# Kernel optimization log

Hardware: AMD Instinct MI355X
Metric: run time of the kernel (lower is better)

The kernel has to match this reference:

```python
import jax, jax.numpy as jnp
import numpy as np

B, N, D, H, WIN = 8, 4096, 768, 8, 8
HD = D // H
FG = N // 2 + 1
FL = WIN // 2 + 1


def _gelu(x):
    return jax.nn.gelu(x, approximate=False)


def _cgelu(z):
    # magnitude-based complex GELU: z * gelu(|z|) / (|z| + 1e-6)
    mag = jnp.abs(z)
    return z * (_gelu(mag) / (mag + 1e-6))


def setup_inputs():
    key = jax.random.key(0)
    ks = jax.random.split(key, 8)

    def w(k, shape):
        return jax.random.normal(k, shape, dtype=jnp.float32) * 0.02

    return {
        "x": jax.random.normal(ks[0], (B, N, D), dtype=jnp.float32),
        "ln_w": jnp.ones((D,), jnp.float32),
        "ln_b": jnp.zeros((D,), jnp.float32),
        "bf_g": jnp.ones((H, FG, 1), jnp.float32),
        "bb_g": jnp.full((H, FG, 1), -0.1, jnp.float32),
        "bf_l": jnp.ones((H, FL, 1), jnp.float32),
        "bb_l": jnp.full((H, FL, 1), -0.1, jnp.float32),
        "w1g": w(ks[1], (D, D)),
        "b1g": jnp.zeros((D,), jnp.float32),
        "w2g": w(ks[2], (D, H * FG * 2)),
        "b2g": jnp.zeros((H * FG * 2,), jnp.float32),
        "w1l": w(ks[3], (D, D)),
        "b1l": jnp.zeros((D,), jnp.float32),
        "w2l": w(ks[4], (D, H * FL * 2)),
        "b2l": jnp.zeros((H * FL * 2,), jnp.float32),
        "wf1": w(ks[5], (D, D // 2)),
        "bf1": jnp.zeros((D // 2,), jnp.float32),
        "wf2": w(ks[6], (D // 2, H)),
        "bf2": jnp.zeros((H,), jnp.float32),
    }


def reference(x, ln_w, ln_b, bf_g, bb_g, bf_l, bb_l, w1g, b1g, w2g, b2g,
              w1l, b1l, w2l, b2l, wf1, bf1, wf2, bf2):
    # pre-norm (LayerNorm, eps=1e-5)
    mu = jnp.mean(x, axis=-1, keepdims=True)
    var = jnp.mean((x - mu) ** 2, axis=-1, keepdims=True)
    xn = (x - mu) / jnp.sqrt(var + 1e-5) * ln_w + ln_b
    xh = xn.reshape(B, N, H, HD).transpose(0, 2, 1, 3)  # (B,H,N,HD)
    ctx = xn.mean(axis=1)  # (B,D)

    # ---- global branch: Hann-windowed rFFT over full sequence ----
    ag = (_gelu(ctx @ w1g + b1g) @ w2g + b2g).reshape(B, H, FG, 2)
    hann_g = jnp.hanning(N).astype(x.dtype)[None, None, :, None]
    Ff = jnp.fft.rfft(xh * hann_g, axis=2, norm="ortho")  # (B,H,FG,HD) complex
    eff_f = bf_g[None] * (1.0 + ag[..., 0:1])
    eff_b = bb_g[None] + ag[..., 1:2]
    x_global = jnp.fft.irfft(_cgelu(Ff * eff_f + eff_b), n=N, axis=2, norm="ortho")

    al = (_gelu(ctx @ w1l + b1l) @ w2l + b2l).reshape(B, H, FL, 2)
    nw = N // WIN
    hann_l = jnp.hanning(WIN).astype(x.dtype)[None, None, None, :, None]
    xw = xh.reshape(B, H, nw, WIN, HD) * hann_l
    Fl_fft = jnp.fft.rfft(xw, axis=3, norm="ortho")  # (B,H,nw,FL,HD)
    eff_fl = bf_l[None, :, None] * (1.0 + al[:, :, None, :, 0:1])
    eff_bl = bb_l[None, :, None] + al[:, :, None, :, 1:2]
    x_local = jnp.fft.irfft(_cgelu(Fl_fft * eff_fl + eff_bl), n=WIN, axis=3,
                            norm="ortho").reshape(B, H, N, HD)

    # ---- fusion gate ----
    alpha = jax.nn.sigmoid(_gelu(ctx @ wf1 + bf1) @ wf2 + bf2).reshape(B, H, 1, 1)
    fused = alpha * x_global + (1.0 - alpha) * x_local
    return x + fused.transpose(0, 2, 1, 3).reshape(B, N, D)
```

## Files before the change

### kernel.cpp

```cpp
#include <hip/hip_runtime.h>
#include <math.h>

#define B_ 8
#define N_ 4096
#define D_ 768
#define H_ 8
#define HD_ 96
#define FG_ 2049
#define TWO_PI 6.283185307179586476925f
#define PAD(i) ((i) + ((i) >> 5))

__device__ __forceinline__ float erf_fast(float x) {
    float ax = fabsf(x);
    float t = __builtin_amdgcn_rcpf(fmaf(0.3275911f, ax, 1.0f));
    float p = fmaf(fmaf(fmaf(fmaf(1.061405429f, t, -1.453152027f), t, 1.421413741f),
                        t, -0.284496736f), t, 0.254829592f) * t;
    float r = 1.0f - p * __expf(-ax * ax);
    return copysignf(r, x);
}

__device__ __forceinline__ float gelu_f(float x) {
    return 0.5f * x * (1.0f + erf_fast(x * 0.7071067811865475f));
}

__device__ __forceinline__ int rev4_12(int x) {
    int r = (int)(__brev((unsigned)x) >> 20);
    return ((r & 0x555) << 1) | ((r >> 1) & 0x555);
}

__global__ void k_init(const float* __restrict__ b2g, const float* __restrict__ b2l,
                       float2* __restrict__ twg, float* __restrict__ hanng,
                       float* __restrict__ ctx, float* __restrict__ ag,
                       float* __restrict__ al) {
    int i = blockIdx.x * 256 + threadIdx.x;
    if (i < 2048) {
        float s, c;
        sincosf(-TWO_PI * (float)i / 4096.0f, &s, &c);
        twg[i] = make_float2(c, s);
    }
    if (i < 4096) hanng[i] = 0.5f - 0.5f * cosf(TWO_PI * (float)i / 4095.0f);
    if (i < B_ * D_) ctx[i] = 0.f;
    const int CG = H_ * FG_ * 2;
    if (i < CG) {
        float v = b2g[i];
        for (int b = 0; b < B_; ++b) ag[(size_t)b * CG + i] = v;
    } else if (i < CG + 80) {
        int cc = i - CG;
        float v = b2l[cc];
        for (int b = 0; b < B_; ++b) al[b * 80 + cc] = v;
    }
}

__global__ __launch_bounds__(256) void k_stats(const float* __restrict__ x,
                                               float* __restrict__ mu,
                                               float* __restrict__ rstd) {
    int row = blockIdx.x * 4 + (threadIdx.x >> 6);
    int lane = threadIdx.x & 63;
    const float4* xr = (const float4*)(x + (size_t)row * D_);
    float4 a = xr[lane], b = xr[lane + 64], c = xr[lane + 128];
    float s = a.x + a.y + a.z + a.w + b.x + b.y + b.z + b.w + c.x + c.y + c.z + c.w;
    #pragma unroll
    for (int o = 32; o > 0; o >>= 1) s += __shfl_xor(s, o);
    float m = s * (1.0f / 768.0f);
    float v = 0.f, d;
    d = a.x - m; v += d * d; d = a.y - m; v += d * d;
    d = a.z - m; v += d * d; d = a.w - m; v += d * d;
    d = b.x - m; v += d * d; d = b.y - m; v += d * d;
    d = b.z - m; v += d * d; d = b.w - m; v += d * d;
    d = c.x - m; v += d * d; d = c.y - m; v += d * d;
    d = c.z - m; v += d * d; d = c.w - m; v += d * d;
    #pragma unroll
    for (int o = 32; o > 0; o >>= 1) v += __shfl_xor(v, o);
    if (lane == 0) {
        mu[row] = m;
        rstd[row] = rsqrtf(v * (1.0f / 768.0f) + 1e-5f);
    }
}

__global__ __launch_bounds__(256) void k_lnT(const float* __restrict__ x,
                                             const float* __restrict__ mu,
                                             const float* __restrict__ rstd,
                                             const float* __restrict__ lw,
                                             const float* __restrict__ lb,
                                             float* __restrict__ xt,
                                             float* __restrict__ ctx) {
    __shared__ float tile[64][65];
    __shared__ float csum[4][64];
    int d0 = blockIdx.x * 64, n0 = blockIdx.y * 64, b = blockIdx.z;
    int c = threadIdx.x & 63, r4 = threadIdx.x >> 6;
    float w = lw[d0 + c], bias = lb[d0 + c];
    float partial = 0.f;
    #pragma unroll
    for (int q = 0; q < 16; ++q) {
        int r = r4 * 16 + q;
        int row = b * N_ + n0 + r;
        float v = (x[(size_t)row * D_ + d0 + c] - mu[row]) * rstd[row] * w + bias;
        tile[r][c] = v;
        partial += v;
    }
    csum[r4][c] = partial;
    __syncthreads();
    if (r4 == 0)
        atomicAdd(ctx + b * D_ + d0 + c,
                  (csum[0][c] + csum[1][c] + csum[2][c] + csum[3][c]) * (1.0f / 4096.0f));
    #pragma unroll
    for (int q = 0; q < 16; ++q) {
        int r = r4 * 16 + q;
        xt[((size_t)b * D_ + d0 + r) * N_ + n0 + c] = tile[c][r];
    }
}

__global__ void k_mlp1(const float* __restrict__ ctx,
                       const float* __restrict__ w1g, const float* __restrict__ b1g,
                       const float* __restrict__ w1l, const float* __restrict__ b1l,
                       const float* __restrict__ wf1, const float* __restrict__ bf1,
                       float* __restrict__ h1g, float* __restrict__ h1l, float* __restrict__ hf) {
    __shared__ float cl[B_ * D_];
    for (int i = threadIdx.x; i < B_ * D_; i += 256) cl[i] = ctx[i];
    __syncthreads();
    int c = blockIdx.x * 256 + threadIdx.x;
    if (c >= 1920) return;
    const float *w, *bias; float* out; int ncol, cc;
    if (c < 768)      { w = w1g; bias = b1g; out = h1g; ncol = 768; cc = c; }
    else if (c < 1536){ w = w1l; bias = b1l; out = h1l; ncol = 768; cc = c - 768; }
    else              { w = wf1; bias = bf1; out = hf;  ncol = 384; cc = c - 1536; }
    float acc[B_];
    #pragma unroll
    for (int b = 0; b < B_; ++b) acc[b] = 0.f;
    for (int d = 0; d < 768; ++d) {
        float wv = w[(size_t)d * ncol + cc];
        #pragma unroll
        for (int b = 0; b < B_; ++b) acc[b] += cl[b * 768 + d] * wv;
    }
    float bv = bias[cc];
    for (int b = 0; b < B_; ++b) out[b * ncol + cc] = gelu_f(acc[b] + bv);
}

__global__ void k_mlp2(const float* __restrict__ h1g, const float* __restrict__ h1l,
                       const float* __restrict__ hf,
                       const float* __restrict__ w2g, const float* __restrict__ w2l,
                       const float* __restrict__ wf2, const float* __restrict__ bf2,
                       float* __restrict__ ag, float* __restrict__ al, float* __restrict__ gate) {
    int kc = blockIdx.y;
    int d0 = kc * 96;
    __shared__ float lg[B_ * 96];
    __shared__ float ll[B_ * 96];
    for (int i = threadIdx.x; i < B_ * 96; i += 256) {
        int bb = i / 96, dd = i % 96;
        lg[i] = h1g[bb * 768 + d0 + dd];
        ll[i] = h1l[bb * 768 + d0 + dd];
    }
    __syncthreads();
    int c = blockIdx.x * 256 + threadIdx.x;
    const int CG = H_ * FG_ * 2;
    float acc[B_];
    #pragma unroll
    for (int b = 0; b < B_; ++b) acc[b] = 0.f;
    if (c < CG) {
        for (int d = 0; d < 96; ++d) {
            float wv = w2g[(size_t)(d0 + d) * CG + c];
            #pragma unroll
            for (int b = 0; b < B_; ++b) acc[b] += lg[b * 96 + d] * wv;
        }
        for (int b = 0; b < B_; ++b) atomicAdd(ag + (size_t)b * CG + c, acc[b]);
    } else if (c < CG + 80) {
        int cc = c - CG;
        for (int d = 0; d < 96; ++d) {
            float wv = w2l[(d0 + d) * 80 + cc];
            #pragma unroll
            for (int b = 0; b < B_; ++b) acc[b] += ll[b * 96 + d] * wv;
        }
        for (int b = 0; b < B_; ++b) atomicAdd(al + b * 80 + cc, acc[b]);
    } else if (c < CG + 88 && kc == 0) {
        int cc = c - CG - 80;
        for (int d = 0; d < 384; ++d) {
            float wv = wf2[d * 8 + cc];
            #pragma unroll
            for (int b = 0; b < B_; ++b) acc[b] += hf[b * 384 + d] * wv;
        }
        for (int b = 0; b < B_; ++b)
            gate[b * 8 + cc] = 1.0f / (1.0f + expf(-(acc[b] + bf2[cc])));
    }
}

template<int LQ>
__device__ __forceinline__ void dif_stage(float2* z, const float2* __restrict__ twg, int t) {
    const int Q = 1 << LQ;
    #pragma unroll
    for (int u = 0; u < 4; ++u) {
        int j = t + (u << 8);
        int pos = j & (Q - 1);
        int i0 = ((j >> LQ) << (LQ + 2)) + pos;
        int p0 = PAD(i0), p1 = PAD(i0 + Q), p2 = PAD(i0 + 2 * Q), p3 = PAD(i0 + 3 * Q);
        float2 a = z[p0], bq = z[p1], c = z[p2], d = z[p3];
        float t0x = a.x + c.x,  t0y = a.y + c.y;
        float t1x = a.x - c.x,  t1y = a.y - c.y;
        float t2x = bq.x + d.x, t2y = bq.y + d.y;
        float t3x = bq.x - d.x, t3y = bq.y - d.y;
        float2 w1 = twg[pos << (10 - LQ)];
        float2 w2 = make_float2(w1.x * w1.x - w1.y * w1.y, 2.f * w1.x * w1.y);
        float2 w3 = make_float2(w1.x * w2.x - w1.y * w2.y, w1.x * w2.y + w1.y * w2.x);
        z[p0] = make_float2(t0x + t2x, t0y + t2y);
        float y1x = t1x + t3y, y1y = t1y - t3x;
        z[p1] = make_float2(y1x * w1.x - y1y * w1.y, y1x * w1.y + y1y * w1.x);
        float y2x = t0x - t2x, y2y = t0y - t2y;
        z[p2] = make_float2(y2x * w2.x - y2y * w2.y, y2x * w2.y + y2y * w2.x);
        float y3x = t1x - t3y, y3y = t1y + t3x;
        z[p3] = make_float2(y3x * w3.x - y3y * w3.y, y3x * w3.y + y3y * w3.x);
    }
}

template<int LQ>
__device__ __forceinline__ void dit_stage(float2* z, const float2* __restrict__ twg, int t) {
    const int Q = 1 << LQ;
    #pragma unroll
    for (int u = 0; u < 4; ++u) {
        int j = t + (u << 8);
        int pos = j & (Q - 1);
        int i0 = ((j >> LQ) << (LQ + 2)) + pos;
        int p0 = PAD(i0), p1 = PAD(i0 + Q), p2 = PAD(i0 + 2 * Q), p3 = PAD(i0 + 3 * Q);
        float2 a = z[p0], bq = z[p1], c = z[p2], d = z[p3];
        float2 w1 = twg[pos << (10 - LQ)];
        w1.y = -w1.y;
        float2 w2 = make_float2(w1.x * w1.x - w1.y * w1.y, 2.f * w1.x * w1.y);
        float2 w3 = make_float2(w1.x * w2.x - w1.y * w2.y, w1.x * w2.y + w1.y * w2.x);
        float2 bh = make_float2(bq.x * w1.x - bq.y * w1.y, bq.x * w1.y + bq.y * w1.x);
        float2 ch = make_float2(c.x * w2.x - c.y * w2.y, c.x * w2.y + c.y * w2.x);
        float2 dh = make_float2(d.x * w3.x - d.y * w3.y, d.x * w3.y + d.y * w3.x);
        float t0x = a.x + ch.x,  t0y = a.y + ch.y;
        float t1x = a.x - ch.x,  t1y = a.y - ch.y;
        float t2x = bh.x + dh.x, t2y = bh.y + dh.y;
        float t3x = bh.x - dh.x, t3y = bh.y - dh.y;
        z[p0] = make_float2(t0x + t2x, t0y + t2y);
        z[p1] = make_float2(t1x - t3y, t1y + t3x);
        z[p2] = make_float2(t0x - t2x, t0y - t2y);
        z[p3] = make_float2(t1x + t3y, t1y - t3x);
    }
}

#define W16C_INIT {1.f, 0.9238795325f, 0.7071067812f, 0.3826834324f, 0.f, \
                   -0.3826834324f, -0.7071067812f, -0.9238795325f, -1.f, -0.9238795325f}
#define W16S_INIT {0.f, -0.3826834324f, -0.7071067812f, -0.9238795325f, -1.f, \
                   -0.9238795325f, -0.7071067812f, -0.3826834324f, 0.f, 0.3826834324f}

__device__ __forceinline__ void fwd16(float2* v) {
    const float WC[10] = W16C_INIT;
    const float WS[10] = W16S_INIT;
    #pragma unroll
    for (int n0 = 0; n0 < 4; ++n0) {
        float2 a = v[n0], b = v[n0 + 4], c = v[n0 + 8], d = v[n0 + 12];
        float t0x = a.x + c.x, t0y = a.y + c.y, t1x = a.x - c.x, t1y = a.y - c.y;
        float t2x = b.x + d.x, t2y = b.y + d.y, t3x = b.x - d.x, t3y = b.y - d.y;
        v[n0] = make_float2(t0x + t2x, t0y + t2y);
        float y1x = t1x + t3y, y1y = t1y - t3x;
        float y2x = t0x - t2x, y2y = t0y - t2y;
        float y3x = t1x - t3y, y3y = t1y + t3x;
        v[n0 + 4]  = make_float2(y1x * WC[n0] - y1y * WS[n0], y1x * WS[n0] + y1y * WC[n0]);
        v[n0 + 8]  = make_float2(y2x * WC[2*n0] - y2y * WS[2*n0], y2x * WS[2*n0] + y2y * WC[2*n0]);
        v[n0 + 12] = make_float2(y3x * WC[3*n0] - y3y * WS[3*n0], y3x * WS[3*n0] + y3y * WC[3*n0]);
    }
    #pragma unroll
    for (int g = 0; g < 4; ++g) {
        float2 a = v[4*g], b = v[4*g+1], c = v[4*g+2], d = v[4*g+3];
        float t0x = a.x + c.x, t0y = a.y + c.y, t1x = a.x - c.x, t1y = a.y - c.y;
        float t2x = b.x + d.x, t2y = b.y + d.y, t3x = b.x - d.x, t3y = b.y - d.y;
        v[4*g]   = make_float2(t0x + t2x, t0y + t2y);
        v[4*g+1] = make_float2(t1x + t3y, t1y - t3x);
        v[4*g+2] = make_float2(t0x - t2x, t0y - t2y);
        v[4*g+3] = make_float2(t1x - t3y, t1y + t3x);
    }
}

__device__ __forceinline__ void inv16(float2* v) {
    const float WC[10] = W16C_INIT;
    const float WS[10] = W16S_INIT;
    #pragma unroll
    for (int g = 0; g < 4; ++g) {
        float2 a = v[4*g], b = v[4*g+1], c = v[4*g+2], d = v[4*g+3];
        float t0x = a.x + c.x, t0y = a.y + c.y, t1x = a.x - c.x, t1y = a.y - c.y;
        float t2x = b.x + d.x, t2y = b.y + d.y, t3x = b.x - d.x, t3y = b.y - d.y;
        v[4*g]   = make_float2(t0x + t2x, t0y + t2y);
        v[4*g+1] = make_float2(t1x - t3y, t1y + t3x);
        v[4*g+2] = make_float2(t0x - t2x, t0y - t2y);
        v[4*g+3] = make_float2(t1x + t3y, t1y - t3x);
    }
    #pragma unroll
    for (int n0 = 0; n0 < 4; ++n0) {
        float2 a = v[n0];
        float2 b0 = v[n0 + 4], c0 = v[n0 + 8], dd = v[n0 + 12];
        float2 b = make_float2(b0.x * WC[n0] + b0.y * WS[n0], b0.y * WC[n0] - b0.x * WS[n0]);
        float2 c = make_float2(c0.x * WC[2*n0] + c0.y * WS[2*n0], c0.y * WC[2*n0] - c0.x * WS[2*n0]);
        float2 d = make_float2(dd.x * WC[3*n0] + dd.y * WS[3*n0], dd.y * WC[3*n0] - dd.x * WS[3*n0]);
        float t0x = a.x + c.x, t0y = a.y + c.y, t1x = a.x - c.x, t1y = a.y - c.y;
        float t2x = b.x + d.x, t2y = b.y + d.y, t3x = b.x - d.x, t3y = b.y - d.y;
        v[n0]      = make_float2(t0x + t2x, t0y + t2y);
        v[n0 + 4]  = make_float2(t1x - t3y, t1y + t3x);
        v[n0 + 8]  = make_float2(t0x - t2x, t0y - t2y);
        v[n0 + 12] = make_float2(t1x + t3y, t1y - t3x);
    }
}

__global__ __launch_bounds__(256) void k_spectral(
        const float* __restrict__ xt,
        const float* __restrict__ ag,
        const float* __restrict__ al,
        const float* __restrict__ gate,
        const float* __restrict__ bf_g, const float* __restrict__ bb_g,
        const float* __restrict__ bf_l, const float* __restrict__ bb_l,
        const float2* __restrict__ twg, const float* __restrict__ hanng,
        float* __restrict__ fused)
{
    __shared__ float2 z[4224];
    int line0 = blockIdx.x * 2;
    int d0 = line0 % 768, b = line0 / 768;
    int h = d0 / HD_;
    int t = threadIdx.x;

    const float* src0 = xt + (size_t)line0 * N_;
    const float* src1 = src0 + N_;
    float raw0[16], raw1[16];
    #pragma unroll
    for (int q = 0; q < 4; ++q) {
        float4 v0 = ((const float4*)src0)[t * 4 + q];
        float4 v1 = ((const float4*)src1)[t * 4 + q];
        raw0[q * 4 + 0] = v0.x; raw0[q * 4 + 1] = v0.y;
        raw0[q * 4 + 2] = v0.z; raw0[q * 4 + 3] = v0.w;
        raw1[q * 4 + 0] = v1.x; raw1[q * 4 + 1] = v1.y;
        raw1[q * 4 + 2] = v1.z; raw1[q * 4 + 3] = v1.w;
    }
    #pragma unroll
    for (int q = 0; q < 4; ++q) {
        float4 hw = ((const float4*)hanng)[t * 4 + q];
        int nb = t * 16 + q * 4;
        z[PAD(nb + 0)] = make_float2(raw0[q * 4 + 0] * hw.x, raw1[q * 4 + 0] * hw.x);
        z[PAD(nb + 1)] = make_float2(raw0[q * 4 + 1] * hw.y, raw1[q * 4 + 1] * hw.y);
        z[PAD(nb + 2)] = make_float2(raw0[q * 4 + 2] * hw.z, raw1[q * 4 + 2] * hw.z);
        z[PAD(nb + 3)] = make_float2(raw0[q * 4 + 3] * hw.w, raw1[q * 4 + 3] * hw.w);
    }

    float alc = gate[b * 8 + h];
    const float* alb = al + b * 80;
    float effl_f[5], effl_b[5];
    #pragma unroll
    for (int f = 0; f < 5; ++f) {
        int idx = h * 5 + f;
        effl_f[f] = bf_l[idx] * (1.0f + alb[idx * 2]);
        effl_b[f] = bb_l[idx] + alb[idx * 2 + 1];
    }
    const float s8 = 0.3535533905932738f;
    const float c7 = 0.7071067811865476f;
    const float cosT[8] = {1.f, c7, 0.f, -c7, -1.f, -c7, 0.f, c7};
    const float sinT[8] = {0.f, c7, 1.f, c7, 0.f, -c7, -1.f, -c7};
    const float hl[8] = {0.f, 0.18825510f, 0.61126047f, 0.95048444f,
                         0.95048444f, 0.61126047f, 0.18825510f, 0.f};
    float xl0[16], xl1[16];
    #pragma unroll
    for (int ln = 0; ln < 2; ++ln) {
        float* rawp = ln ? raw1 : raw0;
        float* xlp  = ln ? xl1 : xl0;
        #pragma unroll
        for (int w2 = 0; w2 < 2; ++w2) {
            float xw[8];
            #pragma unroll
            for (int j = 0; j < 8; ++j) xw[j] = rawp[w2 * 8 + j] * hl[j];
            float Yr[5], Yi[5];
            #pragma unroll
            for (int f = 0; f < 5; ++f) {
                float fr = 0.f, fi = 0.f;
                #pragma unroll
                for (int j = 0; j < 8; ++j) {
                    int k8 = (f * j) & 7;
                    fr += xw[j] * cosT[k8];
                    fi -= xw[j] * sinT[k8];
                }
                fr *= s8; fi *= s8;
                float zr = fr * effl_f[f] + effl_b[f];
                float zi = fi * effl_f[f];
                float mag = sqrtf(zr * zr + zi * zi);
                float g = gelu_f(mag) * __builtin_amdgcn_rcpf(mag + 1e-6f);
                Yr[f] = zr * g; Yi[f] = zi * g;
            }
            #pragma unroll
            for (int j = 0; j < 8; ++j) {
                float acc = Yr[0] + Yr[4] * ((j & 1) ? -1.f : 1.f);
                #pragma unroll
                for (int f = 1; f < 4; ++f) {
                    int k8 = (f * j) & 7;
                    acc += 2.f * (Yr[f] * cosT[k8] - Yi[f] * sinT[k8]);
                }
                xlp[w2 * 8 + j] = acc * s8;
            }
        }
    }

    __syncthreads();
    dif_stage<10>(z, twg, t); __syncthreads();
    dif_stage<8>(z, twg, t);  __syncthreads();
    dif_stage<6>(z, twg, t);  __syncthreads();
    dif_stage<4>(z, twg, t);  __syncthreads();
    {
        float2 v[16];
        #pragma unroll
        for (int i = 0; i < 16; ++i) v[i] = z[PAD(t * 16 + i)];
        fwd16(v);
        #pragma unroll
        for (int i = 0; i < 16; ++i) z[PAD(t * 16 + i)] = v[i];
    }
    __syncthreads();

    const float inv64 = 1.0f / 64.0f;
    const float* agb = ag + (size_t)b * 32784;
    for (int k = t; k < 2048; k += 256) {
        int km = (4096 - k) & 4095;
        int pk = PAD(rev4_12(k)), pm = PAD(rev4_12(km));
        float2 Z = z[pk], Z2 = z[pm];
        float X0r = 0.5f * (Z.x + Z2.x), X0i = 0.5f * (Z.y - Z2.y);
        float X1r = 0.5f * (Z.y + Z2.y), X1i = -0.5f * (Z.x - Z2.x);
        int idx = h * FG_ + k;
        float efff = bf_g[idx] * (1.0f + agb[idx * 2]);
        float effb = bb_g[idx] + agb[idx * 2 + 1];
        float z0r = X0r * inv64 * efff + effb, z0i = X0i * inv64 * efff;
        float m0 = sqrtf(z0r * z0r + z0i * z0i);
        float g0 = gelu_f(m0) * __builtin_amdgcn_rcpf(m0 + 1e-6f);
        float Y0r = z0r * g0, Y0i = z0i * g0;
        float z1r = X1r * inv64 * efff + effb, z1i = X1i * inv64 * efff;
        float m1 = sqrtf(z1r * z1r + z1i * z1i);
        float g1 = gelu_f(m1) * __builtin_amdgcn_rcpf(m1 + 1e-6f);
        float Y1r = z1r * g1, Y1i = z1i * g1;
        z[pk] = make_float2(Y0r - Y1i, Y0i + Y1r);
        if (k) z[pm] = make_float2(Y0r + Y1i, Y1r - Y0i);
    }
    if (t == 0) {
        int pk = PAD(rev4_12(2048));
        float2 Z = z[pk];
        int idx = h * FG_ + 2048;
        float efff = bf_g[idx] * (1.0f + agb[idx * 2]);
        float effb = bb_g[idx] + agb[idx * 2 + 1];
        float z0r = Z.x * inv64 * efff + effb;
        float m0 = fabsf(z0r);
        float Y0r = z0r * (gelu_f(m0) * __builtin_amdgcn_rcpf(m0 + 1e-6f));
        float z1r = Z.y * inv64 * efff + effb;
        float m1 = fabsf(z1r);
        float Y1r = z1r * (gelu_f(m1) * __builtin_amdgcn_rcpf(m1 + 1e-6f));
        z[pk] = make_float2(Y0r, Y1r);
    }
    __syncthreads();

    {
        float2 v[16];
        #pragma unroll
        for (int i = 0; i < 16; ++i) v[i] = z[PAD(t * 16 + i)];
        inv16(v);
        #pragma unroll
        for (int i = 0; i < 16; ++i) z[PAD(t * 16 + i)] = v[i];
    }
    __syncthreads();
    dit_stage<4>(z, twg, t);  __syncthreads();
    dit_stage<6>(z, twg, t);  __syncthreads();
    dit_stage<8>(z, twg, t);  __syncthreads();
    dit_stage<10>(z, twg, t); __syncthreads();

    float* dst0 = fused + (size_t)line0 * N_;
    float* dst1 = dst0 + N_;
    float one_m = 1.0f - alc;
    #pragma unroll
    for (int q = 0; q < 4; ++q) {
        int base = t * 16 + q * 4;
        float2 za = z[PAD(base + 0)], zb = z[PAD(base + 1)];
        float2 zc = z[PAD(base + 2)], zd = z[PAD(base + 3)];
        float4 v0 = make_float4(alc * za.x * inv64 + one_m * xl0[q * 4 + 0],
                                alc * zb.x * inv64 + one_m * xl0[q * 4 + 1],
                                alc * zc.x * inv64 + one_m * xl0[q * 4 + 2],
                                alc * zd.x * inv64 + one_m * xl0[q * 4 + 3]);
        float4 v1 = make_float4(alc * za.y * inv64 + one_m * xl1[q * 4 + 0],
                                alc * zb.y * inv64 + one_m * xl1[q * 4 + 1],
                                alc * zc.y * inv64 + one_m * xl1[q * 4 + 2],
                                alc * zd.y * inv64 + one_m * xl1[q * 4 + 3]);
        ((float4*)dst0)[t * 4 + q] = v0;
        ((float4*)dst1)[t * 4 + q] = v1;
    }
}

__global__ void k_addout(const float* __restrict__ fused, const float* __restrict__ x,
                         float* __restrict__ out) {
    __shared__ float tile[64][65];
    int d0 = blockIdx.x * 64, n0 = blockIdx.y * 64, b = blockIdx.z;
    int c = threadIdx.x & 63, r4 = threadIdx.x >> 6;
    for (int q = 0; q < 16; ++q) {
        int r = r4 * 16 + q;
        tile[r][c] = fused[((size_t)b * D_ + d0 + r) * N_ + n0 + c];
    }
    __syncthreads();
    for (int q = 0; q < 16; ++q) {
        int r = r4 * 16 + q;
        size_t o = ((size_t)b * N_ + n0 + r) * D_ + d0 + c;
        out[o] = x[o] + tile[c][r];
    }
}

extern "C" void kernel_launch(void* const* d_in, const int* in_sizes, int n_in,
                              void* d_out, int out_size, void* d_ws, size_t ws_size,
                              hipStream_t stream) {
    const float* x    = (const float*)d_in[0];
    const float* ln_w = (const float*)d_in[1];
    const float* ln_b = (const float*)d_in[2];
    const float* bf_g = (const float*)d_in[3];
    const float* bb_g = (const float*)d_in[4];
    const float* bf_l = (const float*)d_in[5];
    const float* bb_l = (const float*)d_in[6];
    const float* w1g  = (const float*)d_in[7];
    const float* b1g  = (const float*)d_in[8];
    const float* w2g  = (const float*)d_in[9];
    const float* b2g  = (const float*)d_in[10];
    const float* w1l  = (const float*)d_in[11];
    const float* b1l  = (const float*)d_in[12];
    const float* w2l  = (const float*)d_in[13];
    const float* b2l  = (const float*)d_in[14];
    const float* wf1  = (const float*)d_in[15];
    const float* bf1  = (const float*)d_in[16];
    const float* wf2  = (const float*)d_in[17];
    const float* bf2  = (const float*)d_in[18];
    float* out = (float*)d_out;

    char* ws = (char*)d_ws;
    const size_t big = (size_t)B_ * D_ * N_ * sizeof(float);
    float* XT  = (float*)ws; ws += big;
    float* FU  = (float*)ws; ws += big;
    float* ctx = (float*)ws; ws += (size_t)B_ * D_ * 4;
    float* h1g = (float*)ws; ws += (size_t)B_ * 768 * 4;
    float* h1l = (float*)ws; ws += (size_t)B_ * 768 * 4;
    float* hf  = (float*)ws; ws += (size_t)B_ * 384 * 4;
    float* ag  = (float*)ws; ws += (size_t)B_ * 32784 * 4;
    float* alb = (float*)ws; ws += (size_t)B_ * 80 * 4;
    float* gat = (float*)ws; ws += (size_t)B_ * 8 * 4;
    float2* twg = (float2*)ws; ws += 2048 * sizeof(float2);
    float* hanng = (float*)ws; ws += 4096 * sizeof(float);
    float* mu   = FU;
    float* rstd = FU + 32768;

    k_init<<<129, 256, 0, stream>>>(b2g, b2l, twg, hanng, ctx, ag, alb);
    k_stats<<<8192, 256, 0, stream>>>(x, mu, rstd);
    k_lnT<<<dim3(12, 64, 8), 256, 0, stream>>>(x, mu, rstd, ln_w, ln_b, XT, ctx);
    k_mlp1<<<8, 256, 0, stream>>>(ctx, w1g, b1g, w1l, b1l, wf1, bf1, h1g, h1l, hf);
    k_mlp2<<<dim3(129, 8), 256, 0, stream>>>(h1g, h1l, hf, w2g, w2l, wf2, bf2, ag, alb, gat);
    k_spectral<<<B_ * D_ / 2, 256, 0, stream>>>(XT, ag, alb, gat, bf_g, bb_g, bf_l, bb_l,
                                                twg, hanng, FU);
    k_addout<<<dim3(12, 64, 8), 256, 0, stream>>>(FU, x, out);
}
```

Baseline: 610.7 us.

## Split-K the first MLP layer and switch the FFT to a DIT/DIF XOR-swizzled layout

The first context MLP layer is split over the reduction dimension across 64 blocks with atomic accumulation, replacing a single 8-block launch. Bias init moves to k_init and the GELU moves into k_mlp2's load. The FFT is reordered so the bit-reversal permutation happens at the load and store steps instead of the spectral step: a DIT forward and a DIF inverse. Padded shared-memory indexing is replaced by an XOR swizzle, which shrinks the LDS array. This adds atomics and scattered bit-reversed LDS writes and reads at the load and store steps in exchange for more parallelism in the small MLP.

```diff
diff --git a/kernel.cpp b/kernel.cpp
--- a/kernel.cpp
+++ b/kernel.cpp
@@ -8,7 +8,7 @@
 #define HD_ 96
 #define FG_ 2049
 #define TWO_PI 6.283185307179586476925f
-#define PAD(i) ((i) + ((i) >> 5))
+#define SWZ(i) ((i) ^ (((i) >> 4) & 15))
 
 __device__ __forceinline__ float erf_fast(float x) {
     float ax = fabsf(x);
@@ -29,9 +29,11 @@
 }
 
 __global__ void k_init(const float* __restrict__ b2g, const float* __restrict__ b2l,
+                       const float* __restrict__ b1g, const float* __restrict__ b1l,
                        float2* __restrict__ twg, float* __restrict__ hanng,
                        float* __restrict__ ctx, float* __restrict__ ag,
-                       float* __restrict__ al) {
+                       float* __restrict__ al, float* __restrict__ h1g,
+                       float* __restrict__ h1l) {
     int i = blockIdx.x * 256 + threadIdx.x;
     if (i < 2048) {
         float s, c;
@@ -40,6 +42,13 @@
     }
     if (i < 4096) hanng[i] = 0.5f - 0.5f * cosf(TWO_PI * (float)i / 4095.0f);
     if (i < B_ * D_) ctx[i] = 0.f;
+    if (i < 768) {
+        float vg = b1g[i], vl = b1l[i];
+        for (int b = 0; b < B_; ++b) {
+            h1g[b * 768 + i] = vg;
+            h1l[b * 768 + i] = vl;
+        }
+    }
     const int CG = H_ * FG_ * 2;
     if (i < CG) {
         float v = b2g[i];
@@ -111,29 +120,39 @@
 }
 
 __global__ void k_mlp1(const float* __restrict__ ctx,
-                       const float* __restrict__ w1g, const float* __restrict__ b1g,
-                       const float* __restrict__ w1l, const float* __restrict__ b1l,
+                       const float* __restrict__ w1g, const float* __restrict__ w1l,
                        const float* __restrict__ wf1, const float* __restrict__ bf1,
-                       float* __restrict__ h1g, float* __restrict__ h1l, float* __restrict__ hf) {
-    __shared__ float cl[B_ * D_];
-    for (int i = threadIdx.x; i < B_ * D_; i += 256) cl[i] = ctx[i];
-    __syncthreads();
-    int c = blockIdx.x * 256 + threadIdx.x;
-    if (c >= 1920) return;
-    const float *w, *bias; float* out; int ncol, cc;
-    if (c < 768)      { w = w1g; bias = b1g; out = h1g; ncol = 768; cc = c; }
-    else if (c < 1536){ w = w1l; bias = b1l; out = h1l; ncol = 768; cc = c - 768; }
-    else              { w = wf1; bias = bf1; out = hf;  ncol = 384; cc = c - 1536; }
+                       float* __restrict__ h1g, float* __restrict__ h1l,
+                       float* __restrict__ hf) {
+    int t = threadIdx.x, xb = blockIdx.x, y = blockIdx.y;
     float acc[B_];
     #pragma unroll
     for (int b = 0; b < B_; ++b) acc[b] = 0.f;
-    for (int d = 0; d < 768; ++d) {
-        float wv = w[(size_t)d * ncol + cc];
-        #pragma unroll
-        for (int b = 0; b < B_; ++b) acc[b] += cl[b * 768 + d] * wv;
-    }
-    float bv = bias[cc];
-    for (int b = 0; b < B_; ++b) out[b * ncol + cc] = gelu_f(acc[b] + bv);
+    if (y < 8) {
+        int c = xb * 256 + t;
+        if (c >= 1536) return;
+        const float* w = (c < 768) ? w1g : w1l;
+        float* out = (c < 768) ? h1g : h1l;
+        int cc = (c < 768) ? c : c - 768;
+        int d0 = y * 96;
+        for (int d = 0; d < 96; ++d) {
+            float wv = w[(size_t)(d0 + d) * 768 + cc];
+            #pragma unroll
+            for (int b = 0; b < B_; ++b) acc[b] += ctx[b * 768 + d0 + d] * wv;
+        }
+        for (int b = 0; b < B_; ++b) atomicAdd(out + b * 768 + cc, acc[b]);
+    } else {
+        if (xb < 6) return;
+        int cc = (xb - 6) * 256 + t;
+        if (cc >= 384) return;
+        for (int d = 0; d < 768; ++d) {
+            float wv = wf1[(size_t)d * 384 + cc];
+            #pragma unroll
+            for (int b = 0; b < B_; ++b) acc[b] += ctx[b * 768 + d] * wv;
+        }
+        float bv = bf1[cc];
+        for (int b = 0; b < B_; ++b) hf[b * 384 + cc] = gelu_f(acc[b] + bv);
+    }
 }
 
 __global__ void k_mlp2(const float* __restrict__ h1g, const float* __restrict__ h1l,
@@ -147,8 +166,8 @@
     __shared__ float ll[B_ * 96];
     for (int i = threadIdx.x; i < B_ * 96; i += 256) {
         int bb = i / 96, dd = i % 96;
-        lg[i] = h1g[bb * 768 + d0 + dd];
-        ll[i] = h1l[bb * 768 + d0 + dd];
+        lg[i] = gelu_f(h1g[bb * 768 + d0 + dd]);
+        ll[i] = gelu_f(h1l[bb * 768 + d0 + dd]);
     }
     __syncthreads();
     int c = blockIdx.x * 256 + threadIdx.x;
@@ -184,47 +203,19 @@
 }
 
 template<int LQ>
-__device__ __forceinline__ void dif_stage(float2* z, const float2* __restrict__ twg, int t) {
+__device__ __forceinline__ void dit_stage_f(float2* z, const float2* __restrict__ twg, int t) {
     const int Q = 1 << LQ;
     #pragma unroll
     for (int u = 0; u < 4; ++u) {
         int j = t + (u << 8);
         int pos = j & (Q - 1);
         int i0 = ((j >> LQ) << (LQ + 2)) + pos;
-        int p0 = PAD(i0), p1 = PAD(i0 + Q), p2 = PAD(i0 + 2 * Q), p3 = PAD(i0 + 3 * Q);
-        float2 a = z[p0], bq = z[p1], c = z[p2], d = z[p3];
-        float t0x = a.x + c.x,  t0y = a.y + c.y;
-        float t1x = a.x - c.x,  t1y = a.y - c.y;
-        float t2x = bq.x + d.x, t2y = bq.y + d.y;
-        float t3x = bq.x - d.x, t3y = bq.y - d.y;
+        int p0 = SWZ(i0), p1 = SWZ(i0 + Q), p2 = SWZ(i0 + 2 * Q), p3 = SWZ(i0 + 3 * Q);
+        float2 a = z[p0], b = z[p1], c = z[p2], d = z[p3];
         float2 w1 = twg[pos << (10 - LQ)];
         float2 w2 = make_float2(w1.x * w1.x - w1.y * w1.y, 2.f * w1.x * w1.y);
         float2 w3 = make_float2(w1.x * w2.x - w1.y * w2.y, w1.x * w2.y + w1.y * w2.x);
-        z[p0] = make_float2(t0x + t2x, t0y + t2y);
-        float y1x = t1x + t3y, y1y = t1y - t3x;
-        z[p1] = make_float2(y1x * w1.x - y1y * w1.y, y1x * w1.y + y1y * w1.x);
-        float y2x = t0x - t2x, y2y = t0y - t2y;
-        z[p2] = make_float2(y2x * w2.x - y2y * w2.y, y2x * w2.y + y2y * w2.x);
-        float y3x = t1x - t3y, y3y = t1y + t3x;
-        z[p3] = make_float2(y3x * w3.x - y3y * w3.y, y3x * w3.y + y3y * w3.x);
-    }
-}
-
-template<int LQ>
-__device__ __forceinline__ void dit_stage(float2* z, const float2* __restrict__ twg, int t) {
-    const int Q = 1 << LQ;
-    #pragma unroll
-    for (int u = 0; u < 4; ++u) {
-        int j = t + (u << 8);
-        int pos = j & (Q - 1);
-        int i0 = ((j >> LQ) << (LQ + 2)) + pos;
-        int p0 = PAD(i0), p1 = PAD(i0 + Q), p2 = PAD(i0 + 2 * Q), p3 = PAD(i0 + 3 * Q);
-        float2 a = z[p0], bq = z[p1], c = z[p2], d = z[p3];
-        float2 w1 = twg[pos << (10 - LQ)];
-        w1.y = -w1.y;
-        float2 w2 = make_float2(w1.x * w1.x - w1.y * w1.y, 2.f * w1.x * w1.y);
-        float2 w3 = make_float2(w1.x * w2.x - w1.y * w2.y, w1.x * w2.y + w1.y * w2.x);
-        float2 bh = make_float2(bq.x * w1.x - bq.y * w1.y, bq.x * w1.y + bq.y * w1.x);
+        float2 bh = make_float2(b.x * w1.x - b.y * w1.y, b.x * w1.y + b.y * w1.x);
         float2 ch = make_float2(c.x * w2.x - c.y * w2.y, c.x * w2.y + c.y * w2.x);
         float2 dh = make_float2(d.x * w3.x - d.y * w3.y, d.x * w3.y + d.y * w3.x);
         float t0x = a.x + ch.x,  t0y = a.y + ch.y;
@@ -232,9 +223,37 @@
         float t2x = bh.x + dh.x, t2y = bh.y + dh.y;
         float t3x = bh.x - dh.x, t3y = bh.y - dh.y;
         z[p0] = make_float2(t0x + t2x, t0y + t2y);
-        z[p1] = make_float2(t1x - t3y, t1y + t3x);
+        z[p1] = make_float2(t1x + t3y, t1y - t3x);
         z[p2] = make_float2(t0x - t2x, t0y - t2y);
-        z[p3] = make_float2(t1x + t3y, t1y - t3x);
+        z[p3] = make_float2(t1x - t3y, t1y + t3x);
+    }
+}
+
+template<int LQ>
+__device__ __forceinline__ void dif_stage_i(float2* z, const float2* __restrict__ twg, int t) {
+    const int Q = 1 << LQ;
+    #pragma unroll
+    for (int u = 0; u < 4; ++u) {
+        int j = t + (u << 8);
+        int pos = j & (Q - 1);
+        int i0 = ((j >> LQ) << (LQ + 2)) + pos;
+        int p0 = SWZ(i0), p1 = SWZ(i0 + Q), p2 = SWZ(i0 + 2 * Q), p3 = SWZ(i0 + 3 * Q);
+        float2 a = z[p0], b = z[p1], c = z[p2], d = z[p3];
+        float t0x = a.x + c.x,  t0y = a.y + c.y;
+        float t1x = a.x - c.x,  t1y = a.y - c.y;
+        float t2x = b.x + d.x,  t2y = b.y + d.y;
+        float t3x = b.x - d.x,  t3y = b.y - d.y;
+        float2 w1 = twg[pos << (10 - LQ)];
+        w1.y = -w1.y;
+        float2 w2 = make_float2(w1.x * w1.x - w1.y * w1.y, 2.f * w1.x * w1.y);
+        float2 w3 = make_float2(w1.x * w2.x - w1.y * w2.y, w1.x * w2.y + w1.y * w2.x);
+        z[p0] = make_float2(t0x + t2x, t0y + t2y);
+        float y1x = t1x - t3y, y1y = t1y + t3x;
+        z[p1] = make_float2(y1x * w1.x - y1y * w1.y, y1x * w1.y + y1y * w1.x);
+        float y2x = t0x - t2x, y2y = t0y - t2y;
+        z[p2] = make_float2(y2x * w2.x - y2y * w2.y, y2x * w2.y + y2y * w2.x);
+        float y3x = t1x + t3y, y3y = t1y - t3x;
+        z[p3] = make_float2(y3x * w3.x - y3y * w3.y, y3x * w3.y + y3y * w3.x);
     }
 }
 
@@ -243,22 +262,7 @@
 #define W16S_INIT {0.f, -0.3826834324f, -0.7071067812f, -0.9238795325f, -1.f, \
                    -0.9238795325f, -0.7071067812f, -0.3826834324f, 0.f, 0.3826834324f}
 
-__device__ __forceinline__ void fwd16(float2* v) {
-    const float WC[10] = W16C_INIT;
-    const float WS[10] = W16S_INIT;
-    #pragma unroll
-    for (int n0 = 0; n0 < 4; ++n0) {
-        float2 a = v[n0], b = v[n0 + 4], c = v[n0 + 8], d = v[n0 + 12];
-        float t0x = a.x + c.x, t0y = a.y + c.y, t1x = a.x - c.x, t1y = a.y - c.y;
-        float t2x = b.x + d.x, t2y = b.y + d.y, t3x = b.x - d.x, t3y = b.y - d.y;
-        v[n0] = make_float2(t0x + t2x, t0y + t2y);
-        float y1x = t1x + t3y, y1y = t1y - t3x;
-        float y2x = t0x - t2x, y2y = t0y - t2y;
-        float y3x = t1x - t3y, y3y = t1y + t3x;
-        v[n0 + 4]  = make_float2(y1x * WC[n0] - y1y * WS[n0], y1x * WS[n0] + y1y * WC[n0]);
-        v[n0 + 8]  = make_float2(y2x * WC[2*n0] - y2y * WS[2*n0], y2x * WS[2*n0] + y2y * WC[2*n0]);
-        v[n0 + 12] = make_float2(y3x * WC[3*n0] - y3y * WS[3*n0], y3x * WS[3*n0] + y3y * WC[3*n0]);
-    }
+__device__ __forceinline__ void fwd16_dit(float2* v) {
     #pragma unroll
     for (int g = 0; g < 4; ++g) {
         float2 a = v[4*g], b = v[4*g+1], c = v[4*g+2], d = v[4*g+3];
@@ -269,11 +273,40 @@
         v[4*g+2] = make_float2(t0x - t2x, t0y - t2y);
         v[4*g+3] = make_float2(t1x - t3y, t1y + t3x);
     }
-}
-
-__device__ __forceinline__ void inv16(float2* v) {
     const float WC[10] = W16C_INIT;
     const float WS[10] = W16S_INIT;
+    #pragma unroll
+    for (int m = 0; m < 4; ++m) {
+        float2 a = v[m];
+        float2 b0 = v[m+4], c0 = v[m+8], d0 = v[m+12];
+        float2 b = make_float2(b0.x*WC[m]   - b0.y*WS[m],   b0.x*WS[m]   + b0.y*WC[m]);
+        float2 c = make_float2(c0.x*WC[2*m] - c0.y*WS[2*m], c0.x*WS[2*m] + c0.y*WC[2*m]);
+        float2 d = make_float2(d0.x*WC[3*m] - d0.y*WS[3*m], d0.x*WS[3*m] + d0.y*WC[3*m]);
+        float t0x = a.x + c.x, t0y = a.y + c.y, t1x = a.x - c.x, t1y = a.y - c.y;
+        float t2x = b.x + d.x, t2y = b.y + d.y, t3x = b.x - d.x, t3y = b.y - d.y;
+        v[m]    = make_float2(t0x + t2x, t0y + t2y);
+        v[m+4]  = make_float2(t1x + t3y, t1y - t3x);
+        v[m+8]  = make_float2(t0x - t2x, t0y - t2y);
+        v[m+12] = make_float2(t1x - t3y, t1y + t3x);
+    }
+}
+
+__device__ __forceinline__ void inv16_dif(float2* v) {
+    const float WC[10] = W16C_INIT;
+    const float WS[10] = W16S_INIT;
+    #pragma unroll
+    for (int m = 0; m < 4; ++m) {
+        float2 a = v[m], b = v[m+4], c = v[m+8], d = v[m+12];
+        float t0x = a.x + c.x, t0y = a.y + c.y, t1x = a.x - c.x, t1y = a.y - c.y;
+        float t2x = b.x + d.x, t2y = b.y + d.y, t3x = b.x - d.x, t3y = b.y - d.y;
+        float y1x = t1x - t3y, y1y = t1y + t3x;
+        float y2x = t0x - t2x, y2y = t0y - t2y;
+        float y3x = t1x + t3y, y3y = t1y - t3x;
+        v[m]    = make_float2(t0x + t2x, t0y + t2y);
+        v[m+4]  = make_float2(y1x*WC[m]   + y1y*WS[m],   y1y*WC[m]   - y1x*WS[m]);
+        v[m+8]  = make_float2(y2x*WC[2*m] + y2y*WS[2*m], y2y*WC[2*m] - y2x*WS[2*m]);
+        v[m+12] = make_float2(y3x*WC[3*m] + y3y*WS[3*m], y3y*WC[3*m] - y3x*WS[3*m]);
+    }
     #pragma unroll
     for (int g = 0; g < 4; ++g) {
         float2 a = v[4*g], b = v[4*g+1], c = v[4*g+2], d = v[4*g+3];
@@ -283,20 +316,6 @@
         v[4*g+1] = make_float2(t1x - t3y, t1y + t3x);
         v[4*g+2] = make_float2(t0x - t2x, t0y - t2y);
         v[4*g+3] = make_float2(t1x + t3y, t1y - t3x);
-    }
-    #pragma unroll
-    for (int n0 = 0; n0 < 4; ++n0) {
-        float2 a = v[n0];
-        float2 b0 = v[n0 + 4], c0 = v[n0 + 8], dd = v[n0 + 12];
-        float2 b = make_float2(b0.x * WC[n0] + b0.y * WS[n0], b0.y * WC[n0] - b0.x * WS[n0]);
-        float2 c = make_float2(c0.x * WC[2*n0] + c0.y * WS[2*n0], c0.y * WC[2*n0] - c0.x * WS[2*n0]);
-        float2 d = make_float2(dd.x * WC[3*n0] + dd.y * WS[3*n0], dd.y * WC[3*n0] - dd.x * WS[3*n0]);
-        float t0x = a.x + c.x, t0y = a.y + c.y, t1x = a.x - c.x, t1y = a.y - c.y;
-        float t2x = b.x + d.x, t2y = b.y + d.y, t3x = b.x - d.x, t3y = b.y - d.y;
-        v[n0]      = make_float2(t0x + t2x, t0y + t2y);
-        v[n0 + 4]  = make_float2(t1x - t3y, t1y + t3x);
-        v[n0 + 8]  = make_float2(t0x - t2x, t0y - t2y);
-        v[n0 + 12] = make_float2(t1x + t3y, t1y - t3x);
     }
 }
 
@@ -310,7 +329,7 @@
         const float2* __restrict__ twg, const float* __restrict__ hanng,
         float* __restrict__ fused)
 {
-    __shared__ float2 z[4224];
+    __shared__ float2 z[4096];
     int line0 = blockIdx.x * 2;
     int d0 = line0 % 768, b = line0 / 768;
     int h = d0 / HD_;
@@ -332,10 +351,10 @@
     for (int q = 0; q < 4; ++q) {
         float4 hw = ((const float4*)hanng)[t * 4 + q];
         int nb = t * 16 + q * 4;
-        z[PAD(nb + 0)] = make_float2(raw0[q * 4 + 0] * hw.x, raw1[q * 4 + 0] * hw.x);
-        z[PAD(nb + 1)] = make_float2(raw0[q * 4 + 1] * hw.y, raw1[q * 4 + 1] * hw.y);
-        z[PAD(nb + 2)] = make_float2(raw0[q * 4 + 2] * hw.z, raw1[q * 4 + 2] * hw.z);
-        z[PAD(nb + 3)] = make_float2(raw0[q * 4 + 3] * hw.w, raw1[q * 4 + 3] * hw.w);
+        z[SWZ(rev4_12(nb + 0))] = make_float2(raw0[q*4+0] * hw.x, raw1[q*4+0] * hw.x);
+        z[SWZ(rev4_12(nb + 1))] = make_float2(raw0[q*4+1] * hw.y, raw1[q*4+1] * hw.y);
+        z[SWZ(rev4_12(nb + 2))] = make_float2(raw0[q*4+2] * hw.z, raw1[q*4+2] * hw.z);
+        z[SWZ(rev4_12(nb + 3))] = make_float2(raw0[q*4+3] * hw.w, raw1[q*4+3] * hw.w);
     }
 
     float alc = gate[b * 8 + h];
@@ -394,25 +413,25 @@
     }
 
     __syncthreads();
-    dif_stage<10>(z, twg, t); __syncthreads();
-    dif_stage<8>(z, twg, t);  __syncthreads();
-    dif_stage<6>(z, twg, t);  __syncthreads();
-    dif_stage<4>(z, twg, t);  __syncthreads();
     {
         float2 v[16];
         #pragma unroll
-        for (int i = 0; i < 16; ++i) v[i] = z[PAD(t * 16 + i)];
-        fwd16(v);
+        for (int i = 0; i < 16; ++i) v[i] = z[SWZ(t * 16 + i)];
+        fwd16_dit(v);
         #pragma unroll
-        for (int i = 0; i < 16; ++i) z[PAD(t * 16 + i)] = v[i];
-    }
-    __syncthreads();
+        for (int i = 0; i < 16; ++i) z[SWZ(t * 16 + i)] = v[i];
+    }
+    __syncthreads();
+    dit_stage_f<4>(z, twg, t);  __syncthreads();
+    dit_stage_f<6>(z, twg, t);  __syncthreads();
+    dit_stage_f<8>(z, twg, t);  __syncthreads();
+    dit_stage_f<10>(z, twg, t); __syncthreads();
 
     const float inv64 = 1.0f / 64.0f;
     const float* agb = ag + (size_t)b * 32784;
     for (int k = t; k < 2048; k += 256) {
         int km = (4096 - k) & 4095;
-        int pk = PAD(rev4_12(k)), pm = PAD(rev4_12(km));
+        int pk = SWZ(k), pm = SWZ(km);
         float2 Z = z[pk], Z2 = z[pm];
         float X0r = 0.5f * (Z.x + Z2.x), X0i = 0.5f * (Z.y - Z2.y);
         float X1r = 0.5f * (Z.y + Z2.y), X1i = -0.5f * (Z.x - Z2.x);
@@ -431,7 +450,7 @@
         if (k) z[pm] = make_float2(Y0r + Y1i, Y1r - Y0i);
     }
     if (t == 0) {
-        int pk = PAD(rev4_12(2048));
+        int pk = SWZ(2048);
         float2 Z = z[pk];
         int idx = h * FG_ + 2048;
         float efff = bf_g[idx] * (1.0f + agb[idx * 2]);
@@ -446,19 +465,19 @@
     }
     __syncthreads();
 
+    dif_stage_i<10>(z, twg, t); __syncthreads();
+    dif_stage_i<8>(z, twg, t);  __syncthreads();
+    dif_stage_i<6>(z, twg, t);  __syncthreads();
+    dif_stage_i<4>(z, twg, t);  __syncthreads();
     {
         float2 v[16];
         #pragma unroll
-        for (int i = 0; i < 16; ++i) v[i] = z[PAD(t * 16 + i)];
-        inv16(v);
+        for (int i = 0; i < 16; ++i) v[i] = z[SWZ(t * 16 + i)];
+        inv16_dif(v);
         #pragma unroll
-        for (int i = 0; i < 16; ++i) z[PAD(t * 16 + i)] = v[i];
-    }
-    __syncthreads();
-    dit_stage<4>(z, twg, t);  __syncthreads();
-    dit_stage<6>(z, twg, t);  __syncthreads();
-    dit_stage<8>(z, twg, t);  __syncthreads();
-    dit_stage<10>(z, twg, t); __syncthreads();
+        for (int i = 0; i < 16; ++i) z[SWZ(t * 16 + i)] = v[i];
+    }
+    __syncthreads();
 
     float* dst0 = fused + (size_t)line0 * N_;
     float* dst1 = dst0 + N_;
@@ -466,8 +485,8 @@
     #pragma unroll
     for (int q = 0; q < 4; ++q) {
         int base = t * 16 + q * 4;
-        float2 za = z[PAD(base + 0)], zb = z[PAD(base + 1)];
-        float2 zc = z[PAD(base + 2)], zd = z[PAD(base + 3)];
+        float2 za = z[SWZ(rev4_12(base + 0))], zb = z[SWZ(rev4_12(base + 1))];
+        float2 zc = z[SWZ(rev4_12(base + 2))], zd = z[SWZ(rev4_12(base + 3))];
         float4 v0 = make_float4(alc * za.x * inv64 + one_m * xl0[q * 4 + 0],
                                 alc * zb.x * inv64 + one_m * xl0[q * 4 + 1],
                                 alc * zc.x * inv64 + one_m * xl0[q * 4 + 2],
@@ -538,10 +557,11 @@
     float* mu   = FU;
     float* rstd = FU + 32768;
 
-    k_init<<<129, 256, 0, stream>>>(b2g, b2l, twg, hanng, ctx, ag, alb);
+    k_init<<<129, 256, 0, stream>>>(b2g, b2l, b1g, b1l, twg, hanng, ctx, ag, alb,
+                                    h1g, h1l);
     k_stats<<<8192, 256, 0, stream>>>(x, mu, rstd);
     k_lnT<<<dim3(12, 64, 8), 256, 0, stream>>>(x, mu, rstd, ln_w, ln_b, XT, ctx);
-    k_mlp1<<<8, 256, 0, stream>>>(ctx, w1g, b1g, w1l, b1l, wf1, bf1, h1g, h1l, hf);
+    k_mlp1<<<dim3(8, 9), 256, 0, stream>>>(ctx, w1g, w1l, wf1, bf1, h1g, h1l, hf);
     k_mlp2<<<dim3(129, 8), 256, 0, stream>>>(h1g, h1l, hf, w2g, w2l, wf2, bf2, ag, alb, gat);
     k_spectral<<<B_ * D_ / 2, 256, 0, stream>>>(XT, ag, alb, gat, bf_g, bb_g, bf_l, bb_l,
                                                 twg, hanng, FU);
```

Result: slower. 625.0 us (+2.3%).
